# Optimization experiments

Measured on AMD Instinct MI355X. Metric: run time of the kernel, lower is better.

The kernel has to match this reference:

```python
import jax, jax.numpy as jnp
import numpy as np

N = 100000   # nodes
E = 1600000  # edges
D = 128      # input_dim == hidden_dim
L = 3        # num_layers
G = 256      # graphs in batch
EPS = 1e-5   # BatchNorm eps


def setup_inputs() -> dict:
    key = jax.random.key(0)
    ks = jax.random.split(key, 10)
    x = jax.random.normal(ks[0], (N, D), dtype=jnp.float32)
    edge_index = jax.random.randint(ks[1], (2, E), 0, N, dtype=jnp.int64)
    batch = jnp.sort(jax.random.randint(ks[2], (N,), 0, G, dtype=jnp.int64))
    # stacked per-layer params (all layers are D->D since input_dim==hidden_dim)
    W = jax.random.normal(ks[3], (L, D, D), dtype=jnp.float32) * 0.05
    b = jax.random.normal(ks[4], (L, D), dtype=jnp.float32) * 0.02
    gamma = 1.0 + 0.1 * jax.random.normal(ks[5], (L, D), dtype=jnp.float32)
    beta = 0.1 * jax.random.normal(ks[6], (L, D), dtype=jnp.float32)
    rmean = 0.05 * jax.random.normal(ks[7], (L, D), dtype=jnp.float32)
    rvar = jax.random.uniform(ks[8], (L, D), minval=0.5, maxval=1.5, dtype=jnp.float32)
    return {"x": x, "W": W, "b": b, "gamma": gamma, "beta": beta,
            "rmean": rmean, "rvar": rvar, "edge_index": edge_index, "batch": batch}


def reference(x, W, b, gamma, beta, rmean, rvar, edge_index, batch):
    # --- GCN normalization with self-loops (same for every layer) ---
    src, dst = edge_index[0], edge_index[1]
    loop = jnp.arange(N, dtype=src.dtype)
    s = jnp.concatenate([src, loop])  # [E+N]
    d = jnp.concatenate([dst, loop])
    deg = jax.ops.segment_sum(jnp.ones(E + N, x.dtype), d, num_segments=N)
    dinv = jnp.where(deg > 0, jax.lax.rsqrt(deg), 0.0)
    norm = dinv[s] * dinv[d]  # [E+N]

    h = x
    for i in range(L):
        m = h @ W[i]                                            # [N, D] dense GEMM
        agg = jax.ops.segment_sum(m[s] * norm[:, None], d, num_segments=N)
        h = agg + b[i]
        # BatchNorm1d (inference: running stats), then ReLU; dropout is identity in eval
        h = (h - rmean[i]) * jax.lax.rsqrt(rvar[i] + EPS) * gamma[i] + beta[i]
        h = jax.nn.relu(h)

    # --- global mean / max pooling by graph id ---
    counts = jax.ops.segment_sum(jnp.ones(N, h.dtype), batch, num_segments=G)
    mean_pool = jax.ops.segment_sum(h, batch, num_segments=G) / jnp.maximum(counts, 1.0)[:, None]
    max_pool = jax.ops.segment_max(h, batch, num_segments=G)
    return jnp.concatenate([mean_pool, max_pool], axis=1)  # [G, 2D]
```

## Files before the change

kernel.cpp:

```cpp
#include <hip/hip_runtime.h>
#include <math.h>
#include <float.h>

#define D 128

typedef short short8 __attribute__((ext_vector_type(8)));
typedef float f32x4 __attribute__((ext_vector_type(4)));

__device__ __forceinline__ unsigned int bf16r(float f) {
    unsigned int u = __float_as_uint(f);
    return (u + 0x7fffu + ((u >> 16) & 1u)) >> 16;
}
__device__ __forceinline__ float bf2f(unsigned int lo16) {
    return __uint_as_float(lo16 << 16);
}


__global__ void count_rank_kernel(const int* __restrict__ dst, int* __restrict__ cnt,
                                  int* __restrict__ rank, int E) {
    int base = (blockIdx.x * blockDim.x + threadIdx.x) * 4;
    if (base + 4 <= E) {
        int4 d = *(const int4*)&dst[base];
        int r0 = atomicAdd(&cnt[d.x], 1);
        int r1 = atomicAdd(&cnt[d.y], 1);
        int r2 = atomicAdd(&cnt[d.z], 1);
        int r3 = atomicAdd(&cnt[d.w], 1);
        *(int4*)&rank[base] = make_int4(r0, r1, r2, r3);
    } else if (base < E) {
        for (int e = base; e < E; ++e) rank[e] = atomicAdd(&cnt[dst[e]], 1);
    }
}

__global__ void scan1(const int* __restrict__ cnt, int* __restrict__ rp, int* __restrict__ aux,
                      float* __restrict__ dinv, int n) {
    __shared__ int sh[256];
    int tid = threadIdx.x;
    int base = blockIdx.x * 1024 + tid * 4;
    int v[4]; int s = 0;
#pragma unroll
    for (int i = 0; i < 4; i++) {
        int idx = base + i;
        int t = (idx < n) ? cnt[idx] : 0;
        if (idx < n) dinv[idx] = rsqrtf((float)t + 1.0f);
        v[i] = s; s += t;
    }
    sh[tid] = s; __syncthreads();
    for (int off = 1; off < 256; off <<= 1) {
        int t = (tid >= off) ? sh[tid - off] : 0;
        __syncthreads();
        sh[tid] += t;
        __syncthreads();
    }
    int excl = sh[tid] - s;
#pragma unroll
    for (int i = 0; i < 4; i++) { int idx = base + i; if (idx < n) rp[idx] = excl + v[i]; }
    if (tid == 255) aux[blockIdx.x] = sh[255];
}

__global__ void scan2(int* aux, int nb) {
    __shared__ int sh[256];
    int tid = threadIdx.x;
    int v = (tid < nb) ? aux[tid] : 0;
    sh[tid] = v; __syncthreads();
    for (int off = 1; off < 256; off <<= 1) {
        int t = (tid >= off) ? sh[tid - off] : 0;
        __syncthreads();
        sh[tid] += t;
        __syncthreads();
    }
    if (tid < nb) aux[tid] = sh[tid] - v;
}

__global__ void scan3(int* __restrict__ rp, const int* __restrict__ aux, int n, int E) {
    int base = blockIdx.x * 1024;
    int add = aux[blockIdx.x];
    for (int i = threadIdx.x; i < 1024; i += 256) {
        int idx = base + i;
        if (idx < n) rp[idx] += add;
    }
    if (blockIdx.x == 0 && threadIdx.x == 0) rp[n] = E;
}

__global__ void fill_kernel(const int* __restrict__ src, const int* __restrict__ dst,
                            const int* __restrict__ rp, const int* __restrict__ rank,
                            int* __restrict__ csr, int E) {
    int base = (blockIdx.x * blockDim.x + threadIdx.x) * 4;
    if (base + 4 <= E) {
        int4 d = *(const int4*)&dst[base];
        int4 s = *(const int4*)&src[base];
        int4 r = *(const int4*)&rank[base];
        int p0 = rp[d.x];
        int p1 = rp[d.y];
        int p2 = rp[d.z];
        int p3 = rp[d.w];
        csr[p0 + r.x] = s.x;
        csr[p1 + r.y] = s.y;
        csr[p2 + r.z] = s.z;
        csr[p3 + r.w] = s.w;
    } else if (base < E) {
        for (int e = base; e < E; ++e) csr[rp[dst[e]] + rank[e]] = src[e];
    }
}


__global__ void wprep_kernel(const float* __restrict__ W, const float* __restrict__ b,
                             const float* __restrict__ gamma, const float* __restrict__ beta,
                             const float* __restrict__ rmean, const float* __restrict__ rvar,
                             unsigned short* __restrict__ Wt, float* __restrict__ sc,
                             float* __restrict__ sh, int L_) {
    int t = blockIdx.x * blockDim.x + threadIdx.x;
    int total = L_ * D * D;
    if (t < total) {
        int l = t / (D * D), rem = t % (D * D);
        int r = rem >> 7, k = rem & 127;
        Wt[t] = (unsigned short)bf16r(W[l * D * D + k * D + r]);
    }
    if (t < L_ * D) {
        float inv = rsqrtf(rvar[t] + 1e-5f);
        float s = inv * gamma[t];
        sc[t] = s;
        sh[t] = (b[t] - rmean[t]) * s + beta[t];
    }
}

#define GBM 128
template<bool F32IN>
__global__ __launch_bounds__(512) void gemm_mfma(const void* __restrict__ hin_v,
                                                 const unsigned short* __restrict__ Wt,
                                                 const float* __restrict__ dinv,
                                                 unsigned short* __restrict__ mout, int n) {
    __shared__ short Ah[GBM * 136];
    __shared__ short Wl[D * 136];
    const int tid = threadIdx.x;
    const int row0 = blockIdx.x * GBM;

#pragma unroll
    for (int i = 0; i < 4; ++i) {
        int c = tid + i * 512;
        int r = c >> 4, ck = (c & 15) * 8;
        int grow = row0 + r;
        if (F32IN) {
            const float* xf = (const float*)hin_v;
            float4 va = make_float4(0.f, 0.f, 0.f, 0.f);
            float4 vb = make_float4(0.f, 0.f, 0.f, 0.f);
            if (grow < n) {
                va = *(const float4*)&xf[(size_t)grow * D + ck];
                vb = *(const float4*)&xf[(size_t)grow * D + ck + 4];
            }
            uint4 pk;
            pk.x = bf16r(va.x) | (bf16r(va.y) << 16);
            pk.y = bf16r(va.z) | (bf16r(va.w) << 16);
            pk.z = bf16r(vb.x) | (bf16r(vb.y) << 16);
            pk.w = bf16r(vb.z) | (bf16r(vb.w) << 16);
            *(uint4*)&Ah[r * 136 + ck] = pk;
        } else {
            const unsigned short* hb = (const unsigned short*)hin_v;
            int4 v = make_int4(0, 0, 0, 0);
            if (grow < n) v = *(const int4*)&hb[(size_t)grow * D + ck];
            *(int4*)&Ah[r * 136 + ck] = v;
        }
    }
#pragma unroll
    for (int i = 0; i < 4; ++i) {
        int c = tid + i * 512;
        int r = c >> 4, ck = (c & 15) * 8;
        *(int4*)&Wl[r * 136 + ck] = *(const int4*)&Wt[(size_t)r * D + ck];
    }
    __syncthreads();

    const int wid = tid >> 6;
    const int lane = tid & 63;
    const int lr = lane & 15;
    const int lg = lane >> 4;

    f32x4 acc[8];
#pragma unroll
    for (int fc = 0; fc < 8; ++fc) acc[fc] = (f32x4){0.f, 0.f, 0.f, 0.f};

#pragma unroll
    for (int ks = 0; ks < 4; ++ks) {
        int kb = ks * 32 + lg * 8;
        short8 y = *(const short8*)&Ah[(wid * 16 + lr) * 136 + kb];
#pragma unroll
        for (int fc = 0; fc < 8; ++fc) {
            short8 x = *(const short8*)&Wl[(fc * 16 + lr) * 136 + kb];
            acc[fc] = __builtin_amdgcn_mfma_f32_16x16x32_bf16(x, y, acc[fc], 0, 0, 0);
        }
    }

    int grow = row0 + wid * 16 + lr;
    if (grow < n) {
        float di = dinv[grow];
#pragma unroll
        for (int fc = 0; fc < 8; ++fc) {
            int gcol = fc * 16 + lg * 4;
            uint2 pk;
            pk.x = bf16r(acc[fc][0] * di) | (bf16r(acc[fc][1] * di) << 16);
            pk.y = bf16r(acc[fc][2] * di) | (bf16r(acc[fc][3] * di) << 16);
            *(uint2*)&mout[(size_t)grow * D + gcol] = pk;
        }
    }
}

__global__ __launch_bounds__(256) void agg_bf16(const unsigned int* __restrict__ M,
                                                const int* __restrict__ rp,
                                                const int* __restrict__ csr,
                                                const float* __restrict__ dinv,
                                                const float* __restrict__ sc,
                                                const float* __restrict__ sh,
                                                unsigned int* __restrict__ H, int n) {
    const int wid = threadIdx.x >> 6;
    const int lane = threadIdx.x & 63;
    const int row = blockIdx.x * 4 + wid;
    if (row >= n) return;

    unsigned int u = M[(unsigned)row * 64u + lane];
    float a0 = bf2f(u & 0xffffu);
    float a1 = bf2f(u >> 16);

    int e = rp[row];
    const int end = rp[row + 1];
    const int n16 = (end - e) >> 4;

    if (n16 > 0) {
        int sa[16];
#pragma unroll
        for (int i = 0; i < 16; ++i) sa[i] = csr[e + i];
        for (int it = 0; it < n16; ++it) {
            int sb[16];
            if (it + 1 < n16) {
#pragma unroll
                for (int i = 0; i < 16; ++i) sb[i] = csr[e + 16 + i];
            } else {
#pragma unroll
                for (int i = 0; i < 16; ++i) sb[i] = 0;
            }
            unsigned int g[16];
#pragma unroll
            for (int i = 0; i < 16; ++i) g[i] = M[(unsigned)sa[i] * 64u + lane];
#pragma unroll
            for (int i = 0; i < 16; ++i) {
                a0 += bf2f(g[i] & 0xffffu);
                a1 += bf2f(g[i] >> 16);
            }
#pragma unroll
            for (int i = 0; i < 16; ++i) sa[i] = sb[i];
            e += 16;
        }
    }
    for (; e + 4 <= end; e += 4) {
        int s[4];
#pragma unroll
        for (int i = 0; i < 4; ++i) s[i] = csr[e + i];
        unsigned int g[4];
#pragma unroll
        for (int i = 0; i < 4; ++i) g[i] = M[(unsigned)s[i] * 64u + lane];
#pragma unroll
        for (int i = 0; i < 4; ++i) {
            a0 += bf2f(g[i] & 0xffffu);
            a1 += bf2f(g[i] >> 16);
        }
    }
    for (; e < end; ++e) {
        unsigned int gs = M[(unsigned)csr[e] * 64u + lane];
        a0 += bf2f(gs & 0xffffu);
        a1 += bf2f(gs >> 16);
    }

    float di = dinv[row];
    int c0 = lane * 2;
    float v0 = fmaxf(a0 * di * sc[c0] + sh[c0], 0.f);
    float v1 = fmaxf(a1 * di * sc[c0 + 1] + sh[c0 + 1], 0.f);
    H[(unsigned)row * 64u + lane] = bf16r(v0) | (bf16r(v1) << 16);
}

__global__ void bounds_kernel(const int* __restrict__ batch, int* __restrict__ gstart, int n, int G) {
    int i = blockIdx.x * blockDim.x + threadIdx.x;
    if (i >= n) return;
    int g = batch[i];
    int gp = (i == 0) ? -1 : batch[i - 1];
    for (int gg = gp + 1; gg <= g; ++gg) gstart[gg] = i;
    if (i == n - 1) for (int gg = g + 1; gg <= G; ++gg) gstart[gg] = n;
}

__global__ __launch_bounds__(64) void pool1(const unsigned int* __restrict__ H,
                                            const int* __restrict__ gstart,
                                            float4* __restrict__ pbuf) {
    int g = blockIdx.x, c = blockIdx.y;
    int lane = threadIdx.x;
    int beg = gstart[g], end = gstart[g + 1];
    int len = end - beg;
    int cb = beg + (int)(((long long)len * c) >> 3);
    int ce = beg + (int)(((long long)len * (c + 1)) >> 3);
    float s0 = 0.f, s1 = 0.f, m0 = -INFINITY, m1 = -INFINITY;
    int i = cb;
    for (; i + 2 <= ce; i += 2) {
        unsigned int ua = H[(size_t)i * 64 + lane];
        unsigned int ub = H[(size_t)(i + 1) * 64 + lane];
        float a0 = bf2f(ua & 0xffffu), a1 = bf2f(ua >> 16);
        float b0 = bf2f(ub & 0xffffu), b1 = bf2f(ub >> 16);
        s0 += a0 + b0; s1 += a1 + b1;
        m0 = fmaxf(m0, fmaxf(a0, b0)); m1 = fmaxf(m1, fmaxf(a1, b1));
    }
    for (; i < ce; ++i) {
        unsigned int ua = H[(size_t)i * 64 + lane];
        float a0 = bf2f(ua & 0xffffu), a1 = bf2f(ua >> 16);
        s0 += a0; s1 += a1;
        m0 = fmaxf(m0, a0); m1 = fmaxf(m1, a1);
    }
    pbuf[((size_t)g * 8 + c) * 64 + lane] = make_float4(s0, s1, m0, m1);
}

__global__ __launch_bounds__(64) void pool2(const float4* __restrict__ pbuf,
                                            const int* __restrict__ gstart,
                                            float* __restrict__ out) {
    int g = blockIdx.x;
    int lane = threadIdx.x;
    float s0 = 0.f, s1 = 0.f, m0 = -INFINITY, m1 = -INFINITY;
#pragma unroll
    for (int c = 0; c < 8; ++c) {
        float4 p = pbuf[((size_t)g * 8 + c) * 64 + lane];
        s0 += p.x; s1 += p.y;
        m0 = fmaxf(m0, p.z); m1 = fmaxf(m1, p.w);
    }
    float cnt = fmaxf((float)(gstart[g + 1] - gstart[g]), 1.0f);
    int c0 = lane * 2;
    out[g * (2 * D) + c0] = s0 / cnt;
    out[g * (2 * D) + c0 + 1] = s1 / cnt;
    out[g * (2 * D) + D + c0] = m0;
    out[g * (2 * D) + D + c0 + 1] = m1;
}

extern "C" void kernel_launch(void* const* d_in, const int* in_sizes, int n_in,
                              void* d_out, int out_size, void* d_ws, size_t ws_size,
                              hipStream_t stream) {
    const float* x     = (const float*)d_in[0];
    const float* W     = (const float*)d_in[1];
    const float* b     = (const float*)d_in[2];
    const float* gamma = (const float*)d_in[3];
    const float* beta  = (const float*)d_in[4];
    const float* rmean = (const float*)d_in[5];
    const float* rvar  = (const float*)d_in[6];
    const int*   eidx  = (const int*)d_in[7];
    const int*   batch = (const int*)d_in[8];

    const int N = in_sizes[8];
    const int E = in_sizes[7] / 2;
    const int L = in_sizes[2] / D;
    const int G = out_size / (2 * D);

    const int* esrc = eidx;
    const int* edst = eidx + E;

    size_t off = 0;
    auto carve = [&](size_t bytes) { size_t cur = off; off += (bytes + 255) & ~(size_t)255; return cur; };
    char* base = (char*)d_ws;
    const int nb = (N + 1023) / 1024;

    int*            cnt  = (int*)           (base + carve((size_t)N * 4));
    int*            rp   = (int*)           (base + carve((size_t)(N + 1) * 4));
    int*            aux  = (int*)           (base + carve((size_t)nb * 4));
    float*          dinv = (float*)         (base + carve((size_t)N * 4));
    int*            rank = (int*)           (base + carve((size_t)E * 4));
    int*            csr  = (int*)           (base + carve((size_t)E * 4));
    unsigned short* hbuf = (unsigned short*)(base + carve((size_t)N * D * 2));
    unsigned short* mbuf = (unsigned short*)(base + carve((size_t)N * D * 2));
    unsigned short* Wt   = (unsigned short*)(base + carve((size_t)L * D * D * 2));
    float*          sc   = (float*)         (base + carve((size_t)L * D * 4));
    float*          shb  = (float*)         (base + carve((size_t)L * D * 4));
    int*            gst  = (int*)           (base + carve((size_t)(G + 1) * 4));
    float4*         pbuf = (float4*)        (base + carve((size_t)G * 8 * 64 * 16));
    (void)ws_size;

    hipMemsetAsync(cnt, 0, (size_t)N * 4, stream);

    int e4b = ((E + 3) / 4 + 255) / 256;
    int nbN = (N + 255) / 256;

    count_rank_kernel<<<e4b, 256, 0, stream>>>(edst, cnt, rank, E);
    scan1<<<nb, 256, 0, stream>>>(cnt, rp, aux, dinv, N);
    scan2<<<1, 256, 0, stream>>>(aux, nb);
    scan3<<<nb, 256, 0, stream>>>(rp, aux, N, E);
    fill_kernel<<<e4b, 256, 0, stream>>>(esrc, edst, rp, rank, csr, E);

    wprep_kernel<<<(L * D * D + 255) / 256, 256, 0, stream>>>(W, b, gamma, beta, rmean, rvar,
                                                              Wt, sc, shb, L);

    int gemmb = (N + GBM - 1) / GBM;
    int aggb = (N + 3) / 4;
    for (int l = 0; l < L; ++l) {
        if (l == 0)
            gemm_mfma<true><<<gemmb, 512, 0, stream>>>((const void*)x, Wt, dinv, mbuf, N);
        else
            gemm_mfma<false><<<gemmb, 512, 0, stream>>>((const void*)hbuf, Wt + (size_t)l * D * D, dinv, mbuf, N);
        agg_bf16<<<aggb, 256, 0, stream>>>((const unsigned int*)mbuf, rp, csr, dinv,
                                           sc + l * D, shb + l * D,
                                           (unsigned int*)hbuf, N);
    }

    bounds_kernel<<<nbN, 256, 0, stream>>>(batch, gst, N, G);
    pool1<<<dim3(G, 8), 64, 0, stream>>>((const unsigned int*)hbuf, gst, pbuf);
    pool2<<<G, 64, 0, stream>>>(pbuf, gst, (float*)d_out);
}
```

Measured before the change: 378.7 us.

## Fuse independent prep kernels and overlap CSR fill with layer-0 GEMM

Merges count/rank, weight prep and graph-bounds computation into one launch that partitions its work by block index. Merges the CSR fill with the first-layer GEMM, which reads its A operand straight from global memory instead of staging it in shared memory. This cuts kernel launches and lets independent work run side by side. The cost is extra code paths per block and a different operand-load pattern for the layer-0 GEMM.

```diff
diff --git a/kernel.cpp b/kernel.cpp
--- a/kernel.cpp
+++ b/kernel.cpp
@@ -15,21 +15,52 @@
     return __uint_as_float(lo16 << 16);
 }
 
-
-__global__ void count_rank_kernel(const int* __restrict__ dst, int* __restrict__ cnt,
-                                  int* __restrict__ rank, int E) {
-    int base = (blockIdx.x * blockDim.x + threadIdx.x) * 4;
-    if (base + 4 <= E) {
-        int4 d = *(const int4*)&dst[base];
-        int r0 = atomicAdd(&cnt[d.x], 1);
-        int r1 = atomicAdd(&cnt[d.y], 1);
-        int r2 = atomicAdd(&cnt[d.z], 1);
-        int r3 = atomicAdd(&cnt[d.w], 1);
-        *(int4*)&rank[base] = make_int4(r0, r1, r2, r3);
-    } else if (base < E) {
-        for (int e = base; e < E; ++e) rank[e] = atomicAdd(&cnt[dst[e]], 1);
-    }
-}
+__global__ __launch_bounds__(256) void prep_fused(
+    const int* __restrict__ dst, int* __restrict__ cnt, int* __restrict__ rank, int E,
+    const float* __restrict__ W, const float* __restrict__ b,
+    const float* __restrict__ gamma, const float* __restrict__ beta,
+    const float* __restrict__ rmean, const float* __restrict__ rvar,
+    unsigned short* __restrict__ Wt, float* __restrict__ sc, float* __restrict__ sh, int L_,
+    const int* __restrict__ batch, int* __restrict__ gstart, int n, int G,
+    int cb, int wb) {
+    int blk = blockIdx.x;
+    int tid = threadIdx.x;
+    if (blk < cb) {
+        int base = (blk * 256 + tid) * 4;
+        if (base + 4 <= E) {
+            int4 d = *(const int4*)&dst[base];
+            int r0 = atomicAdd(&cnt[d.x], 1);
+            int r1 = atomicAdd(&cnt[d.y], 1);
+            int r2 = atomicAdd(&cnt[d.z], 1);
+            int r3 = atomicAdd(&cnt[d.w], 1);
+            *(int4*)&rank[base] = make_int4(r0, r1, r2, r3);
+        } else if (base < E) {
+            for (int e = base; e < E; ++e) rank[e] = atomicAdd(&cnt[dst[e]], 1);
+        }
+    } else if (blk < cb + wb) {
+        int t = (blk - cb) * 256 + tid;
+        int total = L_ * D * D;
+        if (t < total) {
+            int l = t / (D * D), rem = t % (D * D);
+            int r = rem >> 7, k = rem & 127;
+            Wt[t] = (unsigned short)bf16r(W[l * D * D + k * D + r]);
+        }
+        if (t < L_ * D) {
+            float inv = rsqrtf(rvar[t] + 1e-5f);
+            float s = inv * gamma[t];
+            sc[t] = s;
+            sh[t] = (b[t] - rmean[t]) * s + beta[t];
+        }
+    } else {
+        int i = (blk - cb - wb) * 256 + tid;
+        if (i >= n) return;
+        int g = batch[i];
+        int gp = (i == 0) ? -1 : batch[i - 1];
+        for (int gg = gp + 1; gg <= g; ++gg) gstart[gg] = i;
+        if (i == n - 1) for (int gg = g + 1; gg <= G; ++gg) gstart[gg] = n;
+    }
+}
+
 
 __global__ void scan1(const int* __restrict__ cnt, int* __restrict__ rp, int* __restrict__ aux,
                       float* __restrict__ dinv, int n) {
@@ -81,49 +112,108 @@
     if (blockIdx.x == 0 && threadIdx.x == 0) rp[n] = E;
 }
 
-__global__ void fill_kernel(const int* __restrict__ src, const int* __restrict__ dst,
-                            const int* __restrict__ rp, const int* __restrict__ rank,
-                            int* __restrict__ csr, int E) {
-    int base = (blockIdx.x * blockDim.x + threadIdx.x) * 4;
-    if (base + 4 <= E) {
-        int4 d = *(const int4*)&dst[base];
-        int4 s = *(const int4*)&src[base];
-        int4 r = *(const int4*)&rank[base];
-        int p0 = rp[d.x];
-        int p1 = rp[d.y];
-        int p2 = rp[d.z];
-        int p3 = rp[d.w];
-        csr[p0 + r.x] = s.x;
-        csr[p1 + r.y] = s.y;
-        csr[p2 + r.z] = s.z;
-        csr[p3 + r.w] = s.w;
-    } else if (base < E) {
-        for (int e = base; e < E; ++e) csr[rp[dst[e]] + rank[e]] = src[e];
-    }
-}
-
-
-__global__ void wprep_kernel(const float* __restrict__ W, const float* __restrict__ b,
-                             const float* __restrict__ gamma, const float* __restrict__ beta,
-                             const float* __restrict__ rmean, const float* __restrict__ rvar,
-                             unsigned short* __restrict__ Wt, float* __restrict__ sc,
-                             float* __restrict__ sh, int L_) {
-    int t = blockIdx.x * blockDim.x + threadIdx.x;
-    int total = L_ * D * D;
-    if (t < total) {
-        int l = t / (D * D), rem = t % (D * D);
-        int r = rem >> 7, k = rem & 127;
-        Wt[t] = (unsigned short)bf16r(W[l * D * D + k * D + r]);
-    }
-    if (t < L_ * D) {
-        float inv = rsqrtf(rvar[t] + 1e-5f);
-        float s = inv * gamma[t];
-        sc[t] = s;
-        sh[t] = (b[t] - rmean[t]) * s + beta[t];
-    }
-}
-
 #define GBM 128
+template<bool F32IN>
+__device__ __forceinline__ void gemm_body_noA(short* Wl, const void* __restrict__ hin_v,
+                                              const unsigned short* __restrict__ Wt,
+                                              const float* __restrict__ dinv,
+                                              unsigned short* __restrict__ mout, int n, int blk) {
+    const int tid = threadIdx.x;
+    const int row0 = blk * GBM;
+
+#pragma unroll
+    for (int i = 0; i < 4; ++i) {
+        int c = tid + i * 512;
+        int r = c >> 4, ck = (c & 15) * 8;
+        *(int4*)&Wl[r * 136 + ck] = *(const int4*)&Wt[(size_t)r * D + ck];
+    }
+    __syncthreads();
+
+    const int wid = tid >> 6;
+    const int lane = tid & 63;
+    const int lr = lane & 15;
+    const int lg = lane >> 4;
+
+    const int grow = row0 + wid * 16 + lr;
+    const bool valid = grow < n;
+
+    f32x4 acc[8];
+#pragma unroll
+    for (int fc = 0; fc < 8; ++fc) acc[fc] = (f32x4){0.f, 0.f, 0.f, 0.f};
+
+#pragma unroll
+    for (int ks = 0; ks < 4; ++ks) {
+        int kb = ks * 32 + lg * 8;
+        short8 y;
+        if (F32IN) {
+            const float* xf = (const float*)hin_v;
+            float4 va = make_float4(0.f, 0.f, 0.f, 0.f);
+            float4 vb = make_float4(0.f, 0.f, 0.f, 0.f);
+            if (valid) {
+                va = *(const float4*)&xf[(size_t)grow * D + kb];
+                vb = *(const float4*)&xf[(size_t)grow * D + kb + 4];
+            }
+            uint4 pk;
+            pk.x = bf16r(va.x) | (bf16r(va.y) << 16);
+            pk.y = bf16r(va.z) | (bf16r(va.w) << 16);
+            pk.z = bf16r(vb.x) | (bf16r(vb.y) << 16);
+            pk.w = bf16r(vb.z) | (bf16r(vb.w) << 16);
+            y = *(short8*)&pk;
+        } else {
+            const unsigned short* hb = (const unsigned short*)hin_v;
+            if (valid) y = *(const short8*)&hb[(size_t)grow * D + kb];
+            else { int4 z = make_int4(0, 0, 0, 0); y = *(short8*)&z; }
+        }
+#pragma unroll
+        for (int fc = 0; fc < 8; ++fc) {
+            short8 x = *(const short8*)&Wl[(fc * 16 + lr) * 136 + kb];
+            acc[fc] = __builtin_amdgcn_mfma_f32_16x16x32_bf16(x, y, acc[fc], 0, 0, 0);
+        }
+    }
+
+    if (valid) {
+        float di = dinv[grow];
+#pragma unroll
+        for (int fc = 0; fc < 8; ++fc) {
+            int gcol = fc * 16 + lg * 4;
+            uint2 pk;
+            pk.x = bf16r(acc[fc][0] * di) | (bf16r(acc[fc][1] * di) << 16);
+            pk.y = bf16r(acc[fc][2] * di) | (bf16r(acc[fc][3] * di) << 16);
+            *(uint2*)&mout[(size_t)grow * D + gcol] = pk;
+        }
+    }
+}
+
+__global__ __launch_bounds__(512) void fused_fill_gemm0(
+    const float* __restrict__ x, const unsigned short* __restrict__ Wt,
+    const float* __restrict__ dinv, unsigned short* __restrict__ mout, int n,
+    const int* __restrict__ src, const int* __restrict__ dst,
+    const int* __restrict__ rp, const int* __restrict__ rank,
+    int* __restrict__ csr, int E, int gemmb) {
+    __shared__ short Wl[D * 136];
+    if ((int)blockIdx.x < gemmb) {
+        gemm_body_noA<true>(Wl, (const void*)x, Wt, dinv, mout, n, blockIdx.x);
+    } else {
+        int gblk = blockIdx.x - gemmb;
+        int base = (gblk * 512 + (int)threadIdx.x) * 4;
+        if (base + 4 <= E) {
+            int4 d = *(const int4*)&dst[base];
+            int4 s = *(const int4*)&src[base];
+            int4 r = *(const int4*)&rank[base];
+            int p0 = rp[d.x];
+            int p1 = rp[d.y];
+            int p2 = rp[d.z];
+            int p3 = rp[d.w];
+            csr[p0 + r.x] = s.x;
+            csr[p1 + r.y] = s.y;
+            csr[p2 + r.z] = s.z;
+            csr[p3 + r.w] = s.w;
+        } else if (base < E) {
+            for (int e = base; e < E; ++e) csr[rp[dst[e]] + rank[e]] = src[e];
+        }
+    }
+}
+
 template<bool F32IN>
 __global__ __launch_bounds__(512) void gemm_mfma(const void* __restrict__ hin_v,
                                                  const unsigned short* __restrict__ Wt,
@@ -274,15 +364,6 @@
     H[(unsigned)row * 64u + lane] = bf16r(v0) | (bf16r(v1) << 16);
 }
 
-__global__ void bounds_kernel(const int* __restrict__ batch, int* __restrict__ gstart, int n, int G) {
-    int i = blockIdx.x * blockDim.x + threadIdx.x;
-    if (i >= n) return;
-    int g = batch[i];
-    int gp = (i == 0) ? -1 : batch[i - 1];
-    for (int gg = gp + 1; gg <= g; ++gg) gstart[gg] = i;
-    if (i == n - 1) for (int gg = g + 1; gg <= G; ++gg) gstart[gg] = n;
-}
-
 __global__ __launch_bounds__(64) void pool1(const unsigned int* __restrict__ H,
                                             const int* __restrict__ gstart,
                                             float4* __restrict__ pbuf) {
@@ -374,31 +455,34 @@
 
     hipMemsetAsync(cnt, 0, (size_t)N * 4, stream);
 
-    int e4b = ((E + 3) / 4 + 255) / 256;
-    int nbN = (N + 255) / 256;
-
-    count_rank_kernel<<<e4b, 256, 0, stream>>>(edst, cnt, rank, E);
+    const int cb = ((E + 3) / 4 + 255) / 256;
+    const int wb = (L * D * D + 255) / 256;
+    const int bb = (N + 255) / 256;
+    const int gemmb = (N + GBM - 1) / GBM;
+    const int fb = ((E + 3) / 4 + 511) / 512;
+    const int aggb = (N + 3) / 4;
+
+    prep_fused<<<cb + wb + bb, 256, 0, stream>>>(edst, cnt, rank, E,
+                                                 W, b, gamma, beta, rmean, rvar,
+                                                 Wt, sc, shb, L,
+                                                 batch, gst, N, G, cb, wb);
     scan1<<<nb, 256, 0, stream>>>(cnt, rp, aux, dinv, N);
     scan2<<<1, 256, 0, stream>>>(aux, nb);
     scan3<<<nb, 256, 0, stream>>>(rp, aux, N, E);
-    fill_kernel<<<e4b, 256, 0, stream>>>(esrc, edst, rp, rank, csr, E);
-
-    wprep_kernel<<<(L * D * D + 255) / 256, 256, 0, stream>>>(W, b, gamma, beta, rmean, rvar,
-                                                              Wt, sc, shb, L);
-
-    int gemmb = (N + GBM - 1) / GBM;
-    int aggb = (N + 3) / 4;
-    for (int l = 0; l < L; ++l) {
-        if (l == 0)
-            gemm_mfma<true><<<gemmb, 512, 0, stream>>>((const void*)x, Wt, dinv, mbuf, N);
-        else
-            gemm_mfma<false><<<gemmb, 512, 0, stream>>>((const void*)hbuf, Wt + (size_t)l * D * D, dinv, mbuf, N);
+
+    fused_fill_gemm0<<<gemmb + fb, 512, 0, stream>>>(x, Wt, dinv, mbuf, N,
+                                                     esrc, edst, rp, rank, csr, E, gemmb);
+    agg_bf16<<<aggb, 256, 0, stream>>>((const unsigned int*)mbuf, rp, csr, dinv,
+                                       sc, shb, (unsigned int*)hbuf, N);
+
+    for (int l = 1; l < L; ++l) {
+        gemm_mfma<false><<<gemmb, 512, 0, stream>>>((const void*)hbuf, Wt + (size_t)l * D * D,
+                                                    dinv, mbuf, N);
         agg_bf16<<<aggb, 256, 0, stream>>>((const unsigned int*)mbuf, rp, csr, dinv,
                                            sc + l * D, shb + l * D,
                                            (unsigned int*)hbuf, N);
     }
 
-    bounds_kernel<<<nbN, 256, 0, stream>>>(batch, gst, N, G);
     pool1<<<dim3(G, 8), 64, 0, stream>>>((const unsigned int*)hbuf, gst, pbuf);
     pool2<<<G, 64, 0, stream>>>(pbuf, gst, (float*)d_out);
 }
```

New measurement: 367.9 us. 1.03x faster.
